# Kernel tuning notes

Hardware: AMD Instinct MI355X
Metric: run time of the kernel (lower is better)

The kernel has to match this reference:

```python
import jax, jax.numpy as jnp
import numpy as np

BINS = 10


def setup_inputs() -> dict:
    key = jax.random.key(0)
    k1, k2 = jax.random.split(key)
    N, C = 4194304, 16
    inputs = jax.random.normal(k1, (N, C), dtype=jnp.float32)
    target = jax.random.randint(k2, (N,), 0, 2, dtype=jnp.int64)
    return {"inputs": inputs, "target": target}


def reference(inputs, target):
    N = inputs.shape[0]
    edges = jnp.arange(BINS + 1, dtype=inputs.dtype) / BINS  # [0, 0.1, ..., 1.0]

    # p_t = softmax(inputs)[i, target_i]
    logp = jax.nn.log_softmax(inputs, axis=1)
    p_t = jnp.take_along_axis(jnp.exp(logp), target[:, None], axis=1)[:, 0]

    # gradient norm g = |p_t - target| (detached in the original)
    g = jnp.abs(jax.lax.stop_gradient(p_t) - target.astype(inputs.dtype))

    # bin index: matches (g >= edges[i]) & (g < edges[i+1]); clip handles g == 1.0
    bin_idx = jnp.clip(jnp.searchsorted(edges, g, side="right") - 1, 0, BINS - 1)

    # per-bin counts via one scatter-add (replaces the per-bin CPU loop)
    counts = jax.ops.segment_sum(jnp.ones_like(g), bin_idx, num_segments=BINS)
    counts = jnp.maximum(counts, 1.0)  # occupied bins always have count >= 1

    # weights[i] = (N / bins) / num_in_bin(i)
    weights = (N / BINS) / counts[bin_idx]

    # weighted cross entropy, summed
    nll = -jnp.take_along_axis(logp, target[:, None], axis=1)[:, 0]
    return jnp.sum(nll * weights)
```

## Files before the change

kernel.cpp:

```cpp
#include <hip/hip_runtime.h>

#define BINS 10

__global__ __launch_bounds__(256) void ghm_main(const float* __restrict__ x,
                                                const int* __restrict__ tgt,
                                                double* __restrict__ g_sum,
                                                unsigned int* __restrict__ g_cnt,
                                                int n_rows) {
    __shared__ double s_sum[BINS];
    __shared__ unsigned int s_cnt[BINS];
    if (threadIdx.x < BINS) { s_sum[threadIdx.x] = 0.0; s_cnt[threadIdx.x] = 0u; }
    __syncthreads();

    const int j = threadIdx.x & 3;
    const int quad = (blockIdx.x * blockDim.x + threadIdx.x) >> 2;
    const int quads_total = (gridDim.x * blockDim.x) >> 2;

    const float edges[BINS + 1] = {0.0f, 0.1f, 0.2f, 0.3f, 0.4f, 0.5f,
                                   0.6f, 0.7f, 0.8f, 0.9f, 1.0f};

    for (int row = quad; row < n_rows; row += quads_total) {
        const float4 v = ((const float4*)x)[row * 4 + j];

        float m = fmaxf(fmaxf(v.x, v.y), fmaxf(v.z, v.w));
        m = fmaxf(m, __shfl_xor(m, 1));
        m = fmaxf(m, __shfl_xor(m, 2));

        float s = expf(v.x - m) + expf(v.y - m) + expf(v.z - m) + expf(v.w - m);
        s += __shfl_xor(s, 1);
        s += __shfl_xor(s, 2);

        if (j == 0) {
            const int t = tgt[row];
            const float xt = (t == 0) ? v.x : ((t == 1) ? v.y : ((t == 2) ? v.z : v.w));
            const float logp = xt - m - logf(s);
            const float p = expf(logp);
            const float g = fabsf(p - (float)t);

            int b = 0;
            #pragma unroll
            for (int k = 1; k <= BINS; ++k) b += (g >= edges[k]) ? 1 : 0;
            if (b > BINS - 1) b = BINS - 1;

            atomicAdd(&s_cnt[b], 1u);
            atomicAdd(&s_sum[b], (double)(-logp));
        }
    }
    __syncthreads();

    if (threadIdx.x < BINS) {
        if (s_cnt[threadIdx.x] != 0u) {
            atomicAdd(&g_cnt[threadIdx.x], s_cnt[threadIdx.x]);
            atomicAdd(&g_sum[threadIdx.x], s_sum[threadIdx.x]);
        }
    }
}

__global__ void ghm_final(const double* __restrict__ g_sum,
                          const unsigned int* __restrict__ g_cnt,
                          float* __restrict__ out, int n_rows) {
    if (threadIdx.x == 0 && blockIdx.x == 0) {
        const double scale = (double)n_rows / (double)BINS;
        double total = 0.0;
        for (int b = 0; b < BINS; ++b) {
            double c = (double)g_cnt[b];
            if (c < 1.0) c = 1.0;
            total += g_sum[b] / c;
        }
        out[0] = (float)(total * scale);
    }
}

extern "C" void kernel_launch(void* const* d_in, const int* in_sizes, int n_in,
                              void* d_out, int out_size, void* d_ws, size_t ws_size,
                              hipStream_t stream) {
    const float* x = (const float*)d_in[0];
    const int* tgt = (const int*)d_in[1];
    const int n_rows = in_sizes[1];

    double* g_sum = (double*)d_ws;
    unsigned int* g_cnt = (unsigned int*)((char*)d_ws + BINS * sizeof(double));

    hipMemsetAsync(d_ws, 0, BINS * (sizeof(double) + sizeof(unsigned int)), stream);

    const int block = 256;
    const int grid = 2048;
    ghm_main<<<grid, block, 0, stream>>>(x, tgt, g_sum, g_cnt, n_rows);
    ghm_final<<<1, 64, 0, stream>>>(g_sum, g_cnt, (float*)d_out, n_rows);
}
```

Before: 401.6 us.

## Process one row per thread with register-private bin histograms

Each thread now processes a whole 16-column row with four float4 loads instead of splitting it across four lanes with shuffles. Per-bin sums and counts are accumulated in registers and flushed to shared memory once per thread, removing per-row shared double atomics. Global bin counters are padded onto separate cache lines. This costs extra registers for the per-bin accumulators and select operations per row.

```diff
diff --git a/kernel.cpp b/kernel.cpp
--- a/kernel.cpp
+++ b/kernel.cpp
@@ -12,46 +12,68 @@
     if (threadIdx.x < BINS) { s_sum[threadIdx.x] = 0.0; s_cnt[threadIdx.x] = 0u; }
     __syncthreads();
 
-    const int j = threadIdx.x & 3;
-    const int quad = (blockIdx.x * blockDim.x + threadIdx.x) >> 2;
-    const int quads_total = (gridDim.x * blockDim.x) >> 2;
-
     const float edges[BINS + 1] = {0.0f, 0.1f, 0.2f, 0.3f, 0.4f, 0.5f,
                                    0.6f, 0.7f, 0.8f, 0.9f, 1.0f};
 
-    for (int row = quad; row < n_rows; row += quads_total) {
-        const float4 v = ((const float4*)x)[row * 4 + j];
+    double acc[BINS];
+    unsigned int cnt[BINS];
+#pragma unroll
+    for (int k = 0; k < BINS; ++k) { acc[k] = 0.0; cnt[k] = 0u; }
 
-        float m = fmaxf(fmaxf(v.x, v.y), fmaxf(v.z, v.w));
-        m = fmaxf(m, __shfl_xor(m, 1));
-        m = fmaxf(m, __shfl_xor(m, 2));
+    const int tid = blockIdx.x * blockDim.x + threadIdx.x;
+    const int nthreads = gridDim.x * blockDim.x;
+    const float4* __restrict__ x4 = (const float4*)x;
 
-        float s = expf(v.x - m) + expf(v.y - m) + expf(v.z - m) + expf(v.w - m);
-        s += __shfl_xor(s, 1);
-        s += __shfl_xor(s, 2);
+    for (int row = tid; row < n_rows; row += nthreads) {
+        const float4 a = x4[row * 4 + 0];
+        const float4 b = x4[row * 4 + 1];
+        const float4 c = x4[row * 4 + 2];
+        const float4 d = x4[row * 4 + 3];
+        const int t = tgt[row];
 
-        if (j == 0) {
-            const int t = tgt[row];
-            const float xt = (t == 0) ? v.x : ((t == 1) ? v.y : ((t == 2) ? v.z : v.w));
-            const float logp = xt - m - logf(s);
-            const float p = expf(logp);
-            const float g = fabsf(p - (float)t);
+        const float m = fmaxf(fmaxf(fmaxf(fmaxf(a.x, a.y), fmaxf(a.z, a.w)),
+                                    fmaxf(fmaxf(b.x, b.y), fmaxf(b.z, b.w))),
+                              fmaxf(fmaxf(fmaxf(c.x, c.y), fmaxf(c.z, c.w)),
+                                    fmaxf(fmaxf(d.x, d.y), fmaxf(d.z, d.w))));
 
-            int b = 0;
-            #pragma unroll
-            for (int k = 1; k <= BINS; ++k) b += (g >= edges[k]) ? 1 : 0;
-            if (b > BINS - 1) b = BINS - 1;
+        const float s0 = expf(a.x - m) + expf(a.y - m) + expf(a.z - m) + expf(a.w - m);
+        const float s1 = expf(b.x - m) + expf(b.y - m) + expf(b.z - m) + expf(b.w - m);
+        const float s2 = expf(c.x - m) + expf(c.y - m) + expf(c.z - m) + expf(c.w - m);
+        const float s3 = expf(d.x - m) + expf(d.y - m) + expf(d.z - m) + expf(d.w - m);
+        const float s = (s0 + s1) + (s2 + s3);
 
-            atomicAdd(&s_cnt[b], 1u);
-            atomicAdd(&s_sum[b], (double)(-logp));
+        const float xt = (t == 0) ? a.x : ((t == 1) ? a.y : ((t == 2) ? a.z : a.w));
+        const float logp = xt - m - logf(s);
+        const float p = expf(logp);
+        const float g = fabsf(p - (float)t);
+
+        int bidx = 0;
+#pragma unroll
+        for (int k = 1; k <= BINS; ++k) bidx += (g >= edges[k]) ? 1 : 0;
+        if (bidx > BINS - 1) bidx = BINS - 1;
+
+        const double nll = (double)(-logp);
+#pragma unroll
+        for (int k = 0; k < BINS; ++k) {
+            const bool h = (bidx == k);
+            acc[k] += h ? nll : 0.0;
+            cnt[k] += h ? 1u : 0u;
+        }
+    }
+
+#pragma unroll
+    for (int k = 0; k < BINS; ++k) {
+        if (cnt[k] != 0u) {
+            atomicAdd(&s_cnt[k], cnt[k]);
+            atomicAdd(&s_sum[k], acc[k]);
         }
     }
     __syncthreads();
 
     if (threadIdx.x < BINS) {
         if (s_cnt[threadIdx.x] != 0u) {
-            atomicAdd(&g_cnt[threadIdx.x], s_cnt[threadIdx.x]);
-            atomicAdd(&g_sum[threadIdx.x], s_sum[threadIdx.x]);
+            atomicAdd(&g_cnt[threadIdx.x * 32], s_cnt[threadIdx.x]);
+            atomicAdd(&g_sum[threadIdx.x * 16], s_sum[threadIdx.x]);
         }
     }
 }
@@ -63,9 +85,9 @@
         const double scale = (double)n_rows / (double)BINS;
         double total = 0.0;
         for (int b = 0; b < BINS; ++b) {
-            double c = (double)g_cnt[b];
+            double c = (double)g_cnt[b * 32];
             if (c < 1.0) c = 1.0;
-            total += g_sum[b] / c;
+            total += g_sum[b * 16] / c;
         }
         out[0] = (float)(total * scale);
     }
@@ -79,9 +101,9 @@
     const int n_rows = in_sizes[1];
 
     double* g_sum = (double*)d_ws;
-    unsigned int* g_cnt = (unsigned int*)((char*)d_ws + BINS * sizeof(double));
+    unsigned int* g_cnt = (unsigned int*)((char*)d_ws + 2048);
 
-    hipMemsetAsync(d_ws, 0, BINS * (sizeof(double) + sizeof(unsigned int)), stream);
+    hipMemsetAsync(d_ws, 0, 4096, stream);
 
     const int block = 256;
     const int grid = 2048;
```

Result: faster. 391.0 us (-2.7%).
